# Kernel tuning notes

Measured on AMD Instinct MI355X. Metric: run time of the kernel, lower is better.

Reference implementation:

```python
import jax, jax.numpy as jnp
import numpy as np

B, S, D_MODEL, D_K, D_V = 4, 2048, 1024, 1024, 1024


def setup_inputs() -> dict:
    key = jax.random.key(0)
    k1, k2, k3, k4 = jax.random.split(key, 4)
    scale = 1.0 / np.sqrt(D_MODEL)
    x = jax.random.normal(k1, (B, S, D_MODEL), dtype=jnp.float32)
    Wq = jax.random.normal(k2, (D_K, D_MODEL), dtype=jnp.float32) * scale
    Wk = jax.random.normal(k3, (D_K, D_MODEL), dtype=jnp.float32) * scale
    Wv = jax.random.normal(k4, (D_V, D_MODEL), dtype=jnp.float32) * scale
    # causal mask: position i may attend to j <= i (True = keep)
    mask = jnp.broadcast_to(jnp.tril(jnp.ones((S, S), dtype=bool)), (B, S, S))
    return {"x": x, "mask": mask, "Wq": Wq, "Wk": Wk, "Wv": Wv}


def reference(x, mask, Wq, Wk, Wv):
    # nn.Linear(d, k, bias=False): y = x @ W.T with W of shape [k, d]
    q = jnp.einsum('bsd,kd->bsk', x, Wq)
    k = jnp.einsum('bsd,kd->bsk', x, Wk)
    v = jnp.einsum('bsd,vd->bsv', x, Wv)
    scores = jnp.einsum('bik,bjk->bij', q, k) / jnp.sqrt(jnp.float32(D_K))
    s = jnp.where(mask, scores, -jnp.inf)
    # masked, fully-masked-row-safe softmax (fully masked rows -> all zeros,
    # matching softmax[all-masked rows] = 0 in the original)
    m = jnp.max(s, axis=-1, keepdims=True)
    m_safe = jnp.where(jnp.isfinite(m), m, 0.0)
    e = jnp.exp(s - m_safe)          # exp(-inf) = 0 for masked entries
    denom = jnp.sum(e, axis=-1, keepdims=True)
    p = e / jnp.where(denom == 0.0, 1.0, denom)
    return jnp.einsum('bij,bjv->biv', p, v)
```

## Files before the change

### kernel.cpp

```cpp
#include <hip/hip_runtime.h>
#include <hip/hip_bf16.h>
#include <stdint.h>

#define SEQ   2048
#define DM    1024
#define NBAT  4

typedef __attribute__((ext_vector_type(8))) short  short8;
typedef __attribute__((ext_vector_type(4))) float  floatx4;

__device__ __forceinline__ unsigned short f2b(float f) {
    __hip_bfloat16 h = __float2bfloat16(f);
    unsigned short r;
    __builtin_memcpy(&r, &h, 2);
    return r;
}

__device__ __forceinline__ ushort4 pack4(float a, float b, float c, float d) {
    ushort4 u; u.x = f2b(a); u.y = f2b(b); u.z = f2b(c); u.w = f2b(d); return u;
}

__device__ __forceinline__ void gload16(const void* g, void* s) {
    __builtin_amdgcn_global_load_lds(
        (const __attribute__((address_space(1))) unsigned int*)(uintptr_t)g,
        (__attribute__((address_space(3))) unsigned int*)(uintptr_t)s,
        16, 0, 0);
}

__global__ void cast_bf16_4(const float4* __restrict__ in, ushort4* __restrict__ out, int n4) {
    int i = blockIdx.x * 256 + threadIdx.x;
    if (i < n4) {
        float4 f = in[i];
        out[i] = pack4(f.x, f.y, f.z, f.w);
    }
}

__global__ void cast_w3(const float4* __restrict__ w0, const float4* __restrict__ w1,
                        const float4* __restrict__ w2, ushort4* __restrict__ out, int n4) {
    const float4* srcs[3] = {w0, w1, w2};
    int i = blockIdx.x * 256 + threadIdx.x;
    if (i < n4) {
        float4 f = srcs[blockIdx.y][i];
        out[(size_t)blockIdx.y * n4 + i] = pack4(f.x, f.y, f.z, f.w);
    }
}

__global__ void zero_u32(unsigned int* __restrict__ p, int n) {
    int i = blockIdx.x * 256 + threadIdx.x;
    if (i < n) p[i] = 0u;
}

__global__ __launch_bounds__(256) void qkv_gemm(
    const unsigned short* __restrict__ A, const unsigned short* __restrict__ Bm,
    unsigned short* __restrict__ Qo, unsigned short* __restrict__ Ko,
    unsigned short* __restrict__ Vto, float qscale)
{
    const int m0 = blockIdx.y * 128;
    const int n0 = blockIdx.x * 128;
    const int K  = DM;
    const bool swapOrd = (n0 < 2048);

    __shared__ __align__(16) unsigned short As[128 * 32];
    __shared__ __align__(16) unsigned short Bs[128 * 32];

    const int t    = threadIdx.x;
    const int w    = t >> 6;
    const int lane = t & 63;
    const int wr   = w >> 1, wc = w & 1;
    const int r    = lane & 15, q = lane >> 4;

    floatx4 acc[4][4];
#pragma unroll
    for (int i = 0; i < 4; i++)
#pragma unroll
        for (int j = 0; j < 4; j++)
            acc[i][j] = (floatx4){0.f, 0.f, 0.f, 0.f};

    const int row0 = t >> 2;
    const int cc0  = t & 3;

    for (int k0 = 0; k0 < K; k0 += 32) {
        const size_t ka = (size_t)k0 + cc0 * 8;
        gload16(A  + (size_t)(m0 + row0)      * K + ka, As + (size_t)w * 512);
        gload16(A  + (size_t)(m0 + row0 + 64) * K + ka, As + 2048 + (size_t)w * 512);
        gload16(Bm + (size_t)(n0 + row0)      * K + ka, Bs + (size_t)w * 512);
        gload16(Bm + (size_t)(n0 + row0 + 64) * K + ka, Bs + 2048 + (size_t)w * 512);
        __builtin_amdgcn_s_waitcnt(0);
        __syncthreads();

        short8 af[4], bf[4];
#pragma unroll
        for (int i = 0; i < 4; i++) {
            af[i] = *(const short8*)&As[(wr * 64 + i * 16 + r) * 32 + q * 8];
            bf[i] = *(const short8*)&Bs[(wc * 64 + i * 16 + r) * 32 + q * 8];
        }
        if (swapOrd) {
#pragma unroll
            for (int i = 0; i < 4; i++)
#pragma unroll
                for (int j = 0; j < 4; j++)
                    acc[i][j] = __builtin_amdgcn_mfma_f32_16x16x32_bf16(bf[j], af[i], acc[i][j], 0, 0, 0);
        } else {
#pragma unroll
            for (int i = 0; i < 4; i++)
#pragma unroll
                for (int j = 0; j < 4; j++)
                    acc[i][j] = __builtin_amdgcn_mfma_f32_16x16x32_bf16(af[i], bf[j], acc[i][j], 0, 0, 0);
        }
        __syncthreads();
    }

    if (swapOrd) {
        const float scale = (n0 < 1024) ? qscale : 1.0f;
        const int gmb = m0 + wr * 64 + r;
        const int gnb = n0 + wc * 64 + q * 4;
#pragma unroll
        for (int i = 0; i < 4; i++) {
            const int gm = gmb + i * 16;
#pragma unroll
            for (int j = 0; j < 4; j++) {
                const int gn = gnb + j * 16;
                ushort4 u = pack4(acc[i][j][0] * scale, acc[i][j][1] * scale,
                                  acc[i][j][2] * scale, acc[i][j][3] * scale);
                if (n0 < 1024)
                    *(ushort4*)&Qo[(size_t)gm * 1024 + gn] = u;
                else
                    *(ushort4*)&Ko[(size_t)gm * 1024 + (gn - 1024)] = u;
            }
        }
    } else {
        const int gmb = m0 + wr * 64 + q * 4;
        const int gnb = n0 + wc * 64 + r;
#pragma unroll
        for (int i = 0; i < 4; i++) {
            const int gm = gmb + i * 16;
            const int b  = gm >> 11;
            const int s  = gm & 2047;
#pragma unroll
            for (int j = 0; j < 4; j++) {
                const int v = gnb + j * 16 - 2048;
                *(ushort4*)&Vto[((size_t)(b * 1024 + v)) * 2048 + s] =
                    pack4(acc[i][j][0], acc[i][j][1], acc[i][j][2], acc[i][j][3]);
            }
        }
    }
}

template<int MODE>
__global__ __launch_bounds__(256) void attn64(
    const unsigned short* __restrict__ Ag, const unsigned short* __restrict__ Bg,
    void* __restrict__ Cv, float* __restrict__ rowsum)
{
    const int z = blockIdx.z;
    int m0, n0;
    if (MODE == 0) {
        const int f = blockIdx.x;
        int ti = (int)((sqrtf(4.f * f + 1.f) - 1.f) * 0.5f);
        while ((ti + 1) * (ti + 2) <= f) ti++;
        while (ti * (ti + 1) > f) ti--;
        const int tj = f - ti * (ti + 1);
        m0 = ti * 128;
        n0 = tj * 64;
    } else {
        m0 = (int)(gridDim.y - 1 - blockIdx.y) * 128;
        n0 = blockIdx.x * 64;
    }

    const int lda = (MODE == 0) ? DM : SEQ;
    const int ldb = (MODE == 0) ? DM : SEQ;
    const unsigned short* A  = Ag + (size_t)z * ((MODE == 0) ? SEQ * DM : SEQ * SEQ);
    const unsigned short* Bm = Bg + (size_t)z * ((MODE == 0) ? SEQ * DM : DM * SEQ);
    const int kEnd = (MODE == 0) ? DM : (m0 + 128);

    __shared__ __align__(16) unsigned short As[128 * 64];
    __shared__ __align__(16) unsigned short Bs[64 * 64];

    const int t    = threadIdx.x;
    const int w    = t >> 6;
    const int lane = t & 63;
    const int r    = lane & 15, q = lane >> 4;

    floatx4 acc[2][4];
#pragma unroll
    for (int i = 0; i < 2; i++)
#pragma unroll
        for (int j = 0; j < 4; j++)
            acc[i][j] = (floatx4){0.f, 0.f, 0.f, 0.f};

    const int rr0 = t >> 3;
    const int pg  = (t & 7) ^ ((t >> 3) & 7);
    const int swz = r & 7;

    for (int k0 = 0; k0 < kEnd; k0 += 64) {
        const size_t ka = (size_t)k0 + pg * 8;
#pragma unroll
        for (int g = 0; g < 4; g++)
            gload16(A + (size_t)(m0 + g * 32 + rr0) * lda + ka,
                    As + g * 2048 + (size_t)w * 512);
#pragma unroll
        for (int g = 0; g < 2; g++)
            gload16(Bm + (size_t)(n0 + g * 32 + rr0) * ldb + ka,
                    Bs + g * 2048 + (size_t)w * 512);
        __builtin_amdgcn_s_waitcnt(0);
        __syncthreads();

#pragma unroll
        for (int kk = 0; kk < 2; kk++) {
            short8 af[2], bf[4];
            const int slot = ((kk * 4 + q) ^ swz) * 8;
#pragma unroll
            for (int i = 0; i < 2; i++)
                af[i] = *(const short8*)&As[(w * 32 + i * 16 + r) * 64 + slot];
#pragma unroll
            for (int j = 0; j < 4; j++)
                bf[j] = *(const short8*)&Bs[(j * 16 + r) * 64 + slot];
#pragma unroll
            for (int i = 0; i < 2; i++)
#pragma unroll
                for (int j = 0; j < 4; j++)
                    acc[i][j] = __builtin_amdgcn_mfma_f32_16x16x32_bf16(bf[j], af[i], acc[i][j], 0, 0, 0);
        }
        __syncthreads();
    }

    const int gmb = m0 + w * 32 + r;
    const int gnb = n0 + q * 4;
    if (MODE == 0) {
        unsigned short* E = (unsigned short*)Cv + (size_t)z * SEQ * SEQ;
        float* rs = rowsum + (size_t)z * SEQ;
#pragma unroll
        for (int i = 0; i < 2; i++) {
            const int gm = gmb + i * 16;
            float part = 0.f;
#pragma unroll
            for (int j = 0; j < 4; j++) {
                const int gn = gnb + j * 16;
                float e0 = (gn + 0 <= gm) ? __expf(acc[i][j][0]) : 0.f;
                float e1 = (gn + 1 <= gm) ? __expf(acc[i][j][1]) : 0.f;
                float e2 = (gn + 2 <= gm) ? __expf(acc[i][j][2]) : 0.f;
                float e3 = (gn + 3 <= gm) ? __expf(acc[i][j][3]) : 0.f;
                part += (e0 + e1) + (e2 + e3);
                *(ushort4*)&E[(size_t)gm * SEQ + gn] = pack4(e0, e1, e2, e3);
            }
            part += __shfl_xor(part, 16, 64);
            part += __shfl_xor(part, 32, 64);
            if (q == 0) atomicAdd(&rs[gm], part);
        }
    } else {
        float* C = (float*)Cv + (size_t)z * SEQ * DM;
        const float* rs = rowsum + (size_t)z * SEQ;
#pragma unroll
        for (int i = 0; i < 2; i++) {
            const int gm = gmb + i * 16;
            const float inv = 1.0f / rs[gm];
#pragma unroll
            for (int j = 0; j < 4; j++) {
                const int gn = gnb + j * 16;
                float4 o;
                o.x = acc[i][j][0] * inv;
                o.y = acc[i][j][1] * inv;
                o.z = acc[i][j][2] * inv;
                o.w = acc[i][j][3] * inv;
                *(float4*)&C[(size_t)gm * DM + gn] = o;
            }
        }
    }
}

extern "C" void kernel_launch(void* const* d_in, const int* in_sizes, int n_in,
                              void* d_out, int out_size, void* d_ws, size_t ws_size,
                              hipStream_t stream) {
    (void)in_sizes; (void)n_in; (void)out_size; (void)ws_size;
    const float* x  = (const float*)d_in[0];
    const float* Wq = (const float*)d_in[2];
    const float* Wk = (const float*)d_in[3];
    const float* Wv = (const float*)d_in[4];

    char* base = (char*)d_ws;
    size_t off = 0;
    auto alloc = [&](size_t n) { char* p = base + off; off += (n + 255) & ~(size_t)255; return p; };

    unsigned short* xb   = (unsigned short*)alloc((size_t)NBAT * SEQ * DM * 2);
    unsigned short* wall = (unsigned short*)alloc((size_t)3 * DM * DM * 2);
    unsigned short* Qb   = (unsigned short*)alloc((size_t)NBAT * SEQ * DM * 2);
    unsigned short* Kb   = (unsigned short*)alloc((size_t)NBAT * SEQ * DM * 2);
    unsigned short* Vtb  = (unsigned short*)alloc((size_t)NBAT * DM * SEQ * 2);
    unsigned short* E    = (unsigned short*)alloc((size_t)NBAT * SEQ * SEQ * 2);
    float*          rsum = (float*)alloc((size_t)NBAT * SEQ * 4);

    const dim3 blk(256);

    {
        int n4 = NBAT * SEQ * DM / 4;
        cast_bf16_4<<<dim3((n4 + 255) / 256), blk, 0, stream>>>((const float4*)x, (ushort4*)xb, n4);
        int w4 = DM * DM / 4;
        cast_w3<<<dim3((w4 + 255) / 256, 3), blk, 0, stream>>>(
            (const float4*)Wq, (const float4*)Wk, (const float4*)Wv, (ushort4*)wall, w4);
        zero_u32<<<dim3((NBAT * SEQ + 255) / 256), blk, 0, stream>>>(
            (unsigned int*)rsum, NBAT * SEQ);
    }

    const int Mtot = NBAT * SEQ;

    qkv_gemm<<<dim3(3 * DM / 128, Mtot / 128, 1), blk, 0, stream>>>(
        xb, wall, Qb, Kb, Vtb, 0.03125f);

    attn64<0><<<dim3(272, 1, NBAT), blk, 0, stream>>>(Qb, Kb, E, rsum);

    attn64<1><<<dim3(DM / 64, SEQ / 128, NBAT), blk, 0, stream>>>(E, Vtb, d_out, rsum);
}
```

Measured before the change: 294.3 us.

## Fuse prep casts into one kernel and deepen QKV GEMM K-tile with swizzled LDS

```diff
diff --git a/kernel.cpp b/kernel.cpp
--- a/kernel.cpp
+++ b/kernel.cpp
@@ -27,27 +27,28 @@
         16, 0, 0);
 }
 
-__global__ void cast_bf16_4(const float4* __restrict__ in, ushort4* __restrict__ out, int n4) {
-    int i = blockIdx.x * 256 + threadIdx.x;
-    if (i < n4) {
-        float4 f = in[i];
-        out[i] = pack4(f.x, f.y, f.z, f.w);
-    }
-}
-
-__global__ void cast_w3(const float4* __restrict__ w0, const float4* __restrict__ w1,
-                        const float4* __restrict__ w2, ushort4* __restrict__ out, int n4) {
-    const float4* srcs[3] = {w0, w1, w2};
-    int i = blockIdx.x * 256 + threadIdx.x;
-    if (i < n4) {
-        float4 f = srcs[blockIdx.y][i];
-        out[(size_t)blockIdx.y * n4 + i] = pack4(f.x, f.y, f.z, f.w);
-    }
-}
-
-__global__ void zero_u32(unsigned int* __restrict__ p, int n) {
-    int i = blockIdx.x * 256 + threadIdx.x;
-    if (i < n) p[i] = 0u;
+__global__ void prep(const float4* __restrict__ x,
+                     const float4* __restrict__ w0, const float4* __restrict__ w1,
+                     const float4* __restrict__ w2,
+                     ushort4* __restrict__ xb, ushort4* __restrict__ wall,
+                     float* __restrict__ rsum)
+{
+    const int b = blockIdx.x;
+    const int t = threadIdx.x;
+    if (b < 8192) {
+        const int i = b * 256 + t;
+        float4 f = x[i];
+        xb[i] = pack4(f.x, f.y, f.z, f.w);
+    } else if (b < 11264) {
+        const int idx  = b - 8192;
+        const int wsel = idx >> 10;
+        const int i    = (idx & 1023) * 256 + t;
+        const float4* src = (wsel == 0) ? w0 : (wsel == 1) ? w1 : w2;
+        float4 f = src[i];
+        wall[(size_t)wsel * 262144 + i] = pack4(f.x, f.y, f.z, f.w);
+    } else {
+        rsum[(b - 11264) * 256 + t] = 0.f;
+    }
 }
 
 __global__ __launch_bounds__(256) void qkv_gemm(
@@ -58,10 +59,9 @@
     const int m0 = blockIdx.y * 128;
     const int n0 = blockIdx.x * 128;
     const int K  = DM;
-    const bool swapOrd = (n0 < 2048);
-
-    __shared__ __align__(16) unsigned short As[128 * 32];
-    __shared__ __align__(16) unsigned short Bs[128 * 32];
+
+    __shared__ __align__(16) unsigned short As[128 * 64];
+    __shared__ __align__(16) unsigned short Bs[128 * 64];
 
     const int t    = threadIdx.x;
     const int w    = t >> 6;
@@ -76,31 +76,29 @@
         for (int j = 0; j < 4; j++)
             acc[i][j] = (floatx4){0.f, 0.f, 0.f, 0.f};
 
-    const int row0 = t >> 2;
-    const int cc0  = t & 3;
-
-    for (int k0 = 0; k0 < K; k0 += 32) {
-        const size_t ka = (size_t)k0 + cc0 * 8;
-        gload16(A  + (size_t)(m0 + row0)      * K + ka, As + (size_t)w * 512);
-        gload16(A  + (size_t)(m0 + row0 + 64) * K + ka, As + 2048 + (size_t)w * 512);
-        gload16(Bm + (size_t)(n0 + row0)      * K + ka, Bs + (size_t)w * 512);
-        gload16(Bm + (size_t)(n0 + row0 + 64) * K + ka, Bs + 2048 + (size_t)w * 512);
+    const int rr0 = t >> 3;
+    const int pg  = (t & 7) ^ ((t >> 3) & 7);
+    const int swz = r & 7;
+
+    for (int k0 = 0; k0 < K; k0 += 64) {
+        const size_t ka = (size_t)k0 + pg * 8;
+#pragma unroll
+        for (int g = 0; g < 4; g++) {
+            gload16(A  + (size_t)(m0 + g * 32 + rr0) * K + ka, As + g * 2048 + (size_t)w * 512);
+            gload16(Bm + (size_t)(n0 + g * 32 + rr0) * K + ka, Bs + g * 2048 + (size_t)w * 512);
+        }
         __builtin_amdgcn_s_waitcnt(0);
         __syncthreads();
 
-        short8 af[4], bf[4];
-#pragma unroll
-        for (int i = 0; i < 4; i++) {
-            af[i] = *(const short8*)&As[(wr * 64 + i * 16 + r) * 32 + q * 8];
-            bf[i] = *(const short8*)&Bs[(wc * 64 + i * 16 + r) * 32 + q * 8];
-        }
-        if (swapOrd) {
-#pragma unroll
-            for (int i = 0; i < 4; i++)
-#pragma unroll
-                for (int j = 0; j < 4; j++)
-                    acc[i][j] = __builtin_amdgcn_mfma_f32_16x16x32_bf16(bf[j], af[i], acc[i][j], 0, 0, 0);
-        } else {
+#pragma unroll
+        for (int kk = 0; kk < 2; kk++) {
+            short8 af[4], bf[4];
+            const int slot = ((kk * 4 + q) ^ swz) * 8;
+#pragma unroll
+            for (int i = 0; i < 4; i++) {
+                af[i] = *(const short8*)&As[(wr * 64 + i * 16 + r) * 64 + slot];
+                bf[i] = *(const short8*)&Bs[(wc * 64 + i * 16 + r) * 64 + slot];
+            }
 #pragma unroll
             for (int i = 0; i < 4; i++)
 #pragma unroll
@@ -110,35 +108,26 @@
         __syncthreads();
     }
 
-    if (swapOrd) {
-        const float scale = (n0 < 1024) ? qscale : 1.0f;
-        const int gmb = m0 + wr * 64 + r;
-        const int gnb = n0 + wc * 64 + q * 4;
-#pragma unroll
-        for (int i = 0; i < 4; i++) {
-            const int gm = gmb + i * 16;
-#pragma unroll
-            for (int j = 0; j < 4; j++) {
-                const int gn = gnb + j * 16;
-                ushort4 u = pack4(acc[i][j][0] * scale, acc[i][j][1] * scale,
-                                  acc[i][j][2] * scale, acc[i][j][3] * scale);
-                if (n0 < 1024)
-                    *(ushort4*)&Qo[(size_t)gm * 1024 + gn] = u;
-                else
-                    *(ushort4*)&Ko[(size_t)gm * 1024 + (gn - 1024)] = u;
-            }
-        }
-    } else {
-        const int gmb = m0 + wr * 64 + q * 4;
-        const int gnb = n0 + wc * 64 + r;
-#pragma unroll
-        for (int i = 0; i < 4; i++) {
-            const int gm = gmb + i * 16;
-            const int b  = gm >> 11;
-            const int s  = gm & 2047;
-#pragma unroll
-            for (int j = 0; j < 4; j++) {
-                const int v = gnb + j * 16 - 2048;
+    const int gmb = m0 + wr * 64 + q * 4;
+    const int gnb = n0 + wc * 64 + r;
+#pragma unroll
+    for (int i = 0; i < 4; i++) {
+        const int gm = gmb + i * 16;
+#pragma unroll
+        for (int j = 0; j < 4; j++) {
+            const int gn = gnb + j * 16;
+            if (n0 < 1024) {
+#pragma unroll
+                for (int rr = 0; rr < 4; rr++)
+                    Qo[(size_t)(gm + rr) * 1024 + gn] = f2b(acc[i][j][rr] * qscale);
+            } else if (n0 < 2048) {
+#pragma unroll
+                for (int rr = 0; rr < 4; rr++)
+                    Ko[(size_t)(gm + rr) * 1024 + (gn - 1024)] = f2b(acc[i][j][rr]);
+            } else {
+                const int b = gm >> 11;
+                const int s = gm & 2047;
+                const int v = gn - 2048;
                 *(ushort4*)&Vto[((size_t)(b * 1024 + v)) * 2048 + s] =
                     pack4(acc[i][j][0], acc[i][j][1], acc[i][j][2], acc[i][j][3]);
             }
@@ -290,15 +279,9 @@
 
     const dim3 blk(256);
 
-    {
-        int n4 = NBAT * SEQ * DM / 4;
-        cast_bf16_4<<<dim3((n4 + 255) / 256), blk, 0, stream>>>((const float4*)x, (ushort4*)xb, n4);
-        int w4 = DM * DM / 4;
-        cast_w3<<<dim3((w4 + 255) / 256, 3), blk, 0, stream>>>(
-            (const float4*)Wq, (const float4*)Wk, (const float4*)Wv, (ushort4*)wall, w4);
-        zero_u32<<<dim3((NBAT * SEQ + 255) / 256), blk, 0, stream>>>(
-            (unsigned int*)rsum, NBAT * SEQ);
-    }
+    prep<<<dim3(11296), blk, 0, stream>>>(
+        (const float4*)x, (const float4*)Wq, (const float4*)Wk, (const float4*)Wv,
+        (ushort4*)xb, (ushort4*)wall, rsum);
 
     const int Mtot = NBAT * SEQ;
 
```

Result: faster. 280.2 us (median of 2 runs) (-4.8%).
